# Optimization experiments

Measured on AMD Instinct MI355X. Metric: run time of the kernel, lower is better.

The kernel has to match this reference:

```python
import jax, jax.numpy as jnp
import numpy as np

K = 20  # hard-coded in Codebook.forward


def _renorm(x):
    # x / ||x||_2 along dim 1, matching torch renorm()
    return x / jnp.linalg.norm(x, axis=1, keepdims=True)


def setup_inputs() -> dict:
    key = jax.random.key(0)
    ks = jax.random.split(key, 6)
    B, N, D = 2048, 50000, 128
    z_rot = jax.random.normal(ks[0], (B, D), dtype=jnp.float32)
    z_trans = jax.random.normal(ks[1], (B, D), dtype=jnp.float32)
    # rotation codebook entries are pre-renormed in create_codetensors
    z_rot_book = _renorm(jax.random.normal(ks[2], (N, D), dtype=jnp.float32))
    z_trans_book = jax.random.normal(ks[3], (N, D), dtype=jnp.float32)
    rot_book = jax.random.uniform(ks[4], (N, 1), dtype=jnp.float32) * 360.0
    trans_book = jax.random.normal(ks[5], (N, 3), dtype=jnp.float32)
    return {
        "z_rot": z_rot,
        "z_trans": z_trans,
        "z_rot_book": z_rot_book,
        "z_trans_book": z_trans_book,
        "rot_book": rot_book,
        "trans_book": trans_book,
    }


def reference(z_rot, z_trans, z_rot_book, z_trans_book, rot_book, trans_book):
    # --- get_nearest_cosine ---
    zr = _renorm(z_rot)                                   # [B, D]
    cos = jnp.einsum("bd,nd->bn", zr, z_rot_book)        # [B, N]
    vals_cos, ind_cos = jax.lax.top_k(cos, K)             # [B, K]
    labels_rot = rot_book[ind_cos]                        # [B, K, 1]

    # --- get_nearest_euclidean ---
    # -(||z - b||^2) = -(||z||^2 - 2 z.b + ||b||^2); avoids the [B,N,D]
    # broadcasted intermediate the torch code materializes (same math).
    zq = jnp.sum(z_trans * z_trans, axis=1, keepdims=True)          # [B, 1]
    bq = jnp.sum(z_trans_book * z_trans_book, axis=1)               # [N]
    m2 = 2.0 * jnp.einsum("bd,nd->bn", z_trans, z_trans_book) - zq - bq[None, :]
    vals_euc, ind_euc = jax.lax.top_k(m2, K)              # [B, K]
    labels_trans = trans_book[ind_euc]                    # [B, K, 3]

    return vals_cos, ind_cos, labels_rot, vals_euc, ind_euc, labels_trans
```

## Files before the change

### kernel.cpp

```cpp
#include <hip/hip_runtime.h>
#include <cfloat>
#include <climits>
#include <math.h>

#define BB 2048
#define NN 50000
#define DD 128
#define KK 20

#define NSLICE 16
#define NSL 3125
#define NTILE 98
#define TAILV 21
#define LK 8
#define SLC 16
#define CAND 256
#define K1W 4

#define O_VC 0
#define O_IC 40960
#define O_LR 81920
#define O_VE 122880
#define O_IE 163840
#define O_LT 204800

#define WS_BBF   0
#define WS_BQ2   25690112
#define WS_CAND  25890112

#define BSTR 132

typedef short v8s __attribute__((ext_vector_type(8)));
typedef float v16f __attribute__((ext_vector_type(16)));

union U4V8 { uint4 u; v8s v; };

__device__ __forceinline__ unsigned int bf16rne(float f) {
    unsigned int x = __float_as_uint(f);
    return (x + 0x7FFFu + ((x >> 16) & 1u)) >> 16;
}
__device__ __forceinline__ unsigned int sortkey(float s) {
    unsigned int b = __float_as_uint(s);
    return b ^ ((unsigned int)((int)b >> 31) | 0x80000000u);
}
__device__ __forceinline__ unsigned int med3u(unsigned int a, unsigned int b, unsigned int c) {
    unsigned int d;
    asm("v_med3_u32 %0, %1, %2, %3" : "=v"(d) : "v"(a), "v"(b), "v"(c));
    return d;
}
__device__ __forceinline__ void ins8(unsigned int (&run)[LK], unsigned int k) {
    #pragma unroll
    for (int u = 0; u < LK - 1; u++) run[u] = med3u(k, run[u], run[u + 1]);
    run[LK - 1] = max(k, run[LK - 1]);
}
__device__ __forceinline__ void ce(unsigned int &a, unsigned int &b) {
    unsigned int lo = min(a, b);
    unsigned int hi = max(a, b);
    a = lo; b = hi;
}
__device__ __forceinline__ void merge8(unsigned int (&run)[LK], const unsigned int* s) {
    unsigned int m[8];
    #pragma unroll
    for (int i = 0; i < 8; i++) m[i] = max(run[i], s[7 - i]);
    ce(m[0],m[4]); ce(m[1],m[5]); ce(m[2],m[6]); ce(m[3],m[7]);
    ce(m[0],m[2]); ce(m[1],m[3]); ce(m[4],m[6]); ce(m[5],m[7]);
    ce(m[0],m[1]); ce(m[2],m[3]); ce(m[4],m[5]); ce(m[6],m[7]);
    #pragma unroll
    for (int i = 0; i < 8; i++) run[i] = m[i];
}

__global__ __launch_bounds__(256) void k_cvt2(const float* __restrict__ bR,
                                              const float* __restrict__ bT,
                                              unsigned int* __restrict__ Bbf,
                                              unsigned int* __restrict__ bq2)
{
    const int tile  = blockIdx.x;
    const int slice = blockIdx.y;
    const int task  = blockIdx.z;
    const int t = threadIdx.x;
    const float* __restrict__ src = task ? bT : bR;
    const float sc = task ? 2.f : 1.f;

    __shared__ float ps[4][64];

    unsigned int* tb = Bbf + (((size_t)(task * NSLICE + slice) * NTILE + tile) << 11);

    float partial = 0.f;
    #pragma unroll
    for (int half = 0; half < 2; half++) {
        const int x = t + half * 256;
        const int c = x & 31, hh = (x >> 5) & 1, q = x >> 6;
        const int es = slice * NSL + min(tile * 32 + c, NSL - 1);
        const float* p = src + (size_t)es * DD + q * 16 + hh * 8;
        float4 u0 = *reinterpret_cast<const float4*>(p);
        float4 u1 = *reinterpret_cast<const float4*>(p + 4);
        partial += u0.x * u0.x + u0.y * u0.y + u0.z * u0.z + u0.w * u0.w
                 + u1.x * u1.x + u1.y * u1.y + u1.z * u1.z + u1.w * u1.w;
        uint4 o;
        o.x = bf16rne(u0.x * sc) | (bf16rne(u0.y * sc) << 16);
        o.y = bf16rne(u0.z * sc) | (bf16rne(u0.w * sc) << 16);
        o.z = bf16rne(u1.x * sc) | (bf16rne(u1.y * sc) << 16);
        o.w = bf16rne(u1.z * sc) | (bf16rne(u1.w * sc) << 16);
        *reinterpret_cast<uint4*>(tb + (q << 8) + hh * 128 + c * 4) = o;
    }

    if (task) {
        ps[t >> 6][t & 63] = partial;
        __syncthreads();
        if (t < 32) {
            float sq = 0.f;
            #pragma unroll
            for (int w2 = 0; w2 < 4; w2++) sq += ps[w2][t] + ps[w2][t + 32];
            unsigned int hi = bf16rne(sq);
            float fhi = __uint_as_float(hi << 16);
            unsigned int lo = bf16rne(sq - fhi);
            const int e = slice * NSL + min(tile * 32 + t, NSL - 1);
            bq2[e] = (hi ^ 0x8000u) | ((lo ^ 0x8000u) << 16);
        }
    }
}

__global__ __launch_bounds__(256, 8) void k1_sel(
    const float* __restrict__ zR, const float* __restrict__ zT,
    const unsigned int* __restrict__ Bbf,
    const unsigned int* __restrict__ bq2,
    uint4* __restrict__ candU)
{
    const int slice = blockIdx.x;
    const int rg    = blockIdx.y;
    const int task  = blockIdx.z;
    const int w     = threadIdx.x >> 6;
    const int lane  = threadIdx.x & 63;
    const int col   = lane & 31;
    const int h     = lane >> 5;

    __shared__ uint4 zs[8][64];
    __shared__ unsigned int smk[K1W - 1][64][LK + 1];

    if (w == 0) {
        const float* zp = (task ? zT : zR) + (size_t)(rg * 32 + col) * DD;
        #pragma unroll
        for (int q = 0; q < 8; q++) {
            float4 u0 = *reinterpret_cast<const float4*>(zp + q * 16 + h * 8);
            float4 u1 = *reinterpret_cast<const float4*>(zp + q * 16 + h * 8 + 4);
            uint4 c;
            c.x = bf16rne(u0.x) | (bf16rne(u0.y) << 16);
            c.y = bf16rne(u0.z) | (bf16rne(u0.w) << 16);
            c.z = bf16rne(u1.x) | (bf16rne(u1.y) << 16);
            c.w = bf16rne(u1.z) | (bf16rne(u1.w) << 16);
            zs[q][lane] = c;
        }
    }
    U4V8 zf8; zf8.u = make_uint4(h == 0 ? 0x3F803F80u : 0u, 0u, 0u, 0u);
    __syncthreads();

    unsigned int run[LK];
    #pragma unroll
    for (int u = 0; u < LK; u++) run[u] = 0u;

    const int nbase0 = slice * NSL;
    const unsigned int* bp = Bbf + ((size_t)(task * NSLICE + slice) * NTILE << 11) + lane * 4;

#define TILE_BODY(TILE, TAIL)                                                          \
    {                                                                                  \
        asm volatile("" ::: "memory");   \
        const unsigned int* tb = bp + ((size_t)(TILE) << 11);                          \
        v16f acc = {0.f,0.f,0.f,0.f, 0.f,0.f,0.f,0.f,                                  \
                    0.f,0.f,0.f,0.f, 0.f,0.f,0.f,0.f};                                 \
        _Pragma("unroll")                                                              \
        for (int q = 0; q < 8; q++) {                                                  \
            U4V8 a; a.u = *reinterpret_cast<const uint4*>(tb + (q << 8));              \
            U4V8 z; z.u = zs[q][lane];                                                 \
            acc = __builtin_amdgcn_mfma_f32_32x32x16_bf16(a.v, z.v, acc, 0, 0, 0);     \
        }                                                                              \
        if (task) {                                                                    \
            int e = nbase0 + (TILE) * 32 + col;                                        \
            if (TAIL) e = min(e, nbase0 + NSL - 1);                                    \
            unsigned int bqp = bq2[e];                                                 \
            U4V8 a; a.u = make_uint4(h == 0 ? bqp : 0u, 0u, 0u, 0u);                   \
            acc = __builtin_amdgcn_mfma_f32_32x32x16_bf16(a.v, zf8.v, acc, 0, 0, 0);   \
        }                                                                              \
        const int nb = nbase0 + (TILE) * 32 + 4 * h;                                   \
        _Pragma("unroll")                                                              \
        for (int r = 0; r < 16; r++) {                                                 \
            const int pat = (r & 3) + 8 * (r >> 2);                                    \
            const int n = nb + pat;                                                    \
            unsigned int k = (sortkey(acc[r]) & 0xFFFF0000u) | (unsigned int)n;        \
            if (TAIL && (pat + 4 * h >= TAILV)) k = 0u;                                \
            ins8(run, k);                                                              \
        }                                                                              \
    }

    int tile = w;
    for (; tile < NTILE - 1; tile += K1W) TILE_BODY(tile, 0)
    if (tile == NTILE - 1) TILE_BODY(tile, 1)
#undef TILE_BODY

    if (w > 0) {
        #pragma unroll
        for (int u = 0; u < LK; u++) smk[w - 1][lane][u] = run[u];
    }
    __syncthreads();
    if (w == 0) {
        #pragma unroll
        for (int v = 0; v < K1W - 1; v++) {
            unsigned int s[LK];
            #pragma unroll
            for (int u = 0; u < LK; u++) s[u] = smk[v][lane][u];
            merge8(run, s);
        }

        uint4 o;
        o.x = (run[0] & 0xFFFFu) | ((run[1] & 0xFFFFu) << 16);
        o.y = (run[2] & 0xFFFFu) | ((run[3] & 0xFFFFu) << 16);
        o.z = (run[4] & 0xFFFFu) | ((run[5] & 0xFFFFu) << 16);
        o.w = (run[6] & 0xFFFFu) | ((run[7] & 0xFFFFu) << 16);
        const int row = rg * 32 + col;
        candU[((size_t)(task * BB + row) * NSLICE + slice) * 2 + h] = o;
    }
}

__global__ __launch_bounds__(256) void k2_final(
    const float* __restrict__ Zr, const float* __restrict__ Zt,
    const float* __restrict__ Br, const float* __restrict__ Bt,
    const float* __restrict__ rotB, const float* __restrict__ transB,
    const unsigned short* __restrict__ candU16,
    float* __restrict__ out)
{
    const int row = blockIdx.x;
    const int task = blockIdx.y;
    const int t = threadIdx.x;
    const float* __restrict__ Z  = task ? Zt : Zr;
    const float* __restrict__ Bk = task ? Bt : Br;

    __shared__ __align__(16) float zrow[DD];
    __shared__ int sel[CAND];
    __shared__ double dsum[CAND];
    __shared__ double sval[KK];
    __shared__ int sidx[KK];
    __shared__ float sv[CAND];
    __shared__ __align__(16) float buf[64 * BSTR];

    if (t < DD) zrow[t] = Z[(size_t)row * DD + t];
    sel[t] = (int)candU16[((size_t)task * BB + row) * CAND + t];
    __syncthreads();

    const int sr = t >> 2;
    const int sg = t & 3;

    for (int c = 0; c < 4; ++c) {
        {
            const int n = sel[c * 64 + sr];
            const float* src = Bk + (size_t)n * DD + sg * 32;
            float4 tmp[8];
            #pragma unroll
            for (int i = 0; i < 8; i++)
                tmp[i] = *reinterpret_cast<const float4*>(src + i * 4);
            #pragma unroll
            for (int i = 0; i < 8; i++)
                *reinterpret_cast<float4*>(&buf[sr * BSTR + sg * 32 + i * 4]) = tmp[i];
        }
        __syncthreads();

        if (task == 0) {
            #pragma unroll
            for (int sub = 0; sub < 2; sub++) {
                const int idx = c * 512 + sub * 256 + t;
                const int cnd = idx >> 3, part = idx & 7;
                const float* brow = &buf[(cnd - c * 64) * BSTR + part * 16];
                double dp = 0.0;
                #pragma unroll
                for (int q = 0; q < 4; q++) {
                    float4 b4 = *reinterpret_cast<const float4*>(brow + q * 4);
                    const int k = part * 16 + q * 4;
                    dp += (double)zrow[k + 0] * (double)b4.x + (double)zrow[k + 1] * (double)b4.y
                        + (double)zrow[k + 2] * (double)b4.z + (double)zrow[k + 3] * (double)b4.w;
                }
                dp += __shfl_xor(dp, 1, 64);
                dp += __shfl_xor(dp, 2, 64);
                dp += __shfl_xor(dp, 4, 64);
                if ((t & 7) == 0) dsum[cnd] = dp;
            }
        } else {
            const float* brow = &buf[sr * BSTR];
            float L = 0.f, rA = 0.f, rB = 0.f, qA = 0.f, qB = 0.f;
            #pragma unroll
            for (int c4 = 0; c4 < 32; c4++) {
                const float b = brow[c4 * 4 + sg];
                const float z = zrow[c4 * 4 + sg];
                L = __fadd_rn(L, __fmul_rn(z, b));
                if ((c4 & 1) == 0) {
                    rA = __fadd_rn(rA, __fmul_rn(b, b));
                    qA = __fadd_rn(qA, __fmul_rn(z, z));
                } else {
                    rB = __fadd_rn(rB, __fmul_rn(b, b));
                    qB = __fadd_rn(qB, __fmul_rn(z, z));
                }
            }
            float a2 = __fadd_rn(L, __shfl_xor(L, 2, 64));
            float dot = __fadd_rn(a2, __shfl_xor(a2, 1, 64));
            float s1 = __fadd_rn(rA, __shfl_xor(rA, 1, 64));
            float u1 = __fadd_rn(s1, __shfl_xor(s1, 2, 64));
            float s2 = __fadd_rn(rB, __shfl_xor(rB, 1, 64));
            float u2 = __fadd_rn(s2, __shfl_xor(s2, 2, 64));
            const float bqv = __fadd_rn(u1, u2);
            float s3 = __fadd_rn(qA, __shfl_xor(qA, 1, 64));
            float u3 = __fadd_rn(s3, __shfl_xor(s3, 2, 64));
            float s4 = __fadd_rn(qB, __shfl_xor(qB, 1, 64));
            float u4 = __fadd_rn(s4, __shfl_xor(s4, 2, 64));
            const float zqv = __fadd_rn(u3, u4);
            if (sg == 0)
                sv[c * 64 + sr] = __fsub_rn(__fsub_rn(__fmul_rn(2.0f, dot), zqv), bqv);
        }
        __syncthreads();
    }

    if (task == 0) {
        if (t < 64) {
            double zq = (double)zrow[t] * (double)zrow[t]
                      + (double)zrow[t + 64] * (double)zrow[t + 64];
            #pragma unroll
            for (int m = 1; m < 64; m <<= 1) zq += __shfl_xor(zq, m, 64);

            double s[4]; int ix[4];
            #pragma unroll
            for (int j = 0; j < 4; j++) {
                const int cc = t + 64 * j;
                s[j] = dsum[cc]; ix[j] = sel[cc];
            }

            for (int rd = 0; rd < KK; rd++) {
                double bs = s[0]; int bn = ix[0];
                #pragma unroll
                for (int j = 1; j < 4; j++)
                    if (s[j] > bs || (s[j] == bs && ix[j] < bn)) { bs = s[j]; bn = ix[j]; }
                #pragma unroll
                for (int m = 1; m < 64; m <<= 1) {
                    double os = __shfl_xor(bs, m, 64);
                    int on = __shfl_xor(bn, m, 64);
                    if (os > bs || (os == bs && on < bn)) { bs = os; bn = on; }
                }
                #pragma unroll
                for (int j = 0; j < 4; j++) if (ix[j] == bn) s[j] = -DBL_MAX;
                if (t == 0) { sval[rd] = bs; sidx[rd] = bn; }
            }
            if (t == 0) dsum[0] = zq;
        }
        __syncthreads();

        if (t < KK) {
            const double zq = dsum[0];
            const int n = sidx[t];
            const int o = row * KK + t;
            out[O_VC + o] = (float)(sval[t] / sqrt(zq));
            out[O_IC + o] = (float)n;
            out[O_LR + o] = rotB[n];
        }
    } else {
        if (t < 64) {
            float s[4]; int ix[4];
            #pragma unroll
            for (int j = 0; j < 4; j++) { s[j] = sv[t + 64 * j]; ix[j] = sel[t + 64 * j]; }

            for (int rd = 0; rd < KK; rd++) {
                float bs = s[0]; int bn = ix[0];
                #pragma unroll
                for (int j = 1; j < 4; j++)
                    if (s[j] > bs || (s[j] == bs && ix[j] < bn)) { bs = s[j]; bn = ix[j]; }
                #pragma unroll
                for (int m = 1; m < 64; m <<= 1) {
                    float os = __shfl_xor(bs, m, 64);
                    int on = __shfl_xor(bn, m, 64);
                    if (os > bs || (os == bs && on < bn)) { bs = os; bn = on; }
                }
                #pragma unroll
                for (int j = 0; j < 4; j++) if (ix[j] == bn) s[j] = -FLT_MAX;
                if (t == 0) {
                    const int o = row * KK + rd;
                    out[O_VE + o] = bs;
                    out[O_IE + o] = (float)bn;
                    const int o3 = O_LT + o * 3;
                    out[o3 + 0] = transB[bn * 3 + 0];
                    out[o3 + 1] = transB[bn * 3 + 1];
                    out[o3 + 2] = transB[bn * 3 + 2];
                }
            }
        }
    }
}

extern "C" void kernel_launch(void* const* d_in, const int* in_sizes, int n_in,
                              void* d_out, int out_size, void* d_ws, size_t ws_size,
                              hipStream_t stream) {
    const float* zR = (const float*)d_in[0];
    const float* zT = (const float*)d_in[1];
    const float* bR = (const float*)d_in[2];
    const float* bT = (const float*)d_in[3];
    const float* rotB = (const float*)d_in[4];
    const float* transB = (const float*)d_in[5];
    float* out = (float*)d_out;

    char* ws = (char*)d_ws;
    unsigned int* Bbf = (unsigned int*)(ws + WS_BBF);
    unsigned int* bq2 = (unsigned int*)(ws + WS_BQ2);
    uint4* candU = (uint4*)(ws + WS_CAND);

    k_cvt2<<<dim3(NTILE, NSLICE, 2), 256, 0, stream>>>(bR, bT, Bbf, bq2);
    k1_sel<<<dim3(NSLICE, 64, 2), 256, 0, stream>>>(zR, zT, Bbf, bq2, candU);
    k2_final<<<dim3(BB, 2), 256, 0, stream>>>(zR, zT, bR, bT, rotB, transB,
                                              (const unsigned short*)candU, out);
}
```

Baseline: 335.4 us.

## Split final rescoring into parallel rescore kernel and wave-sized top-K kernel

Replaces the single per-row final kernel with two kernels. The first rescores the 256 candidates per row across four blocks per row, reading codebook rows straight from global memory with no shared-memory staging or barriers. The second uses one 64-thread wave per row to pick the top-K from the rescored values kept in workspace. This is meant to raise parallelism and remove the serialized chunk loop and its syncs, at the cost of an extra launch and a global round trip for the scores. The scores go in the workspace region that held the bf16 codebook, which is dead by then.

```diff
diff --git a/kernel.cpp b/kernel.cpp
--- a/kernel.cpp
+++ b/kernel.cpp
@@ -27,8 +27,8 @@
 #define WS_BBF   0
 #define WS_BQ2   25690112
 #define WS_CAND  25890112
-
-#define BSTR 132
+#define WS_DSUM  0
+#define WS_SV    4194304
 
 typedef short v8s __attribute__((ext_vector_type(8)));
 typedef float v16f __attribute__((ext_vector_type(16)));
@@ -220,136 +220,119 @@
     }
 }
 
-__global__ __launch_bounds__(256) void k2_final(
+__global__ __launch_bounds__(256) void k2a_rescore(
     const float* __restrict__ Zr, const float* __restrict__ Zt,
     const float* __restrict__ Br, const float* __restrict__ Bt,
+    const unsigned short* __restrict__ candU16,
+    double* __restrict__ dsumW, float* __restrict__ svW)
+{
+    const int row   = blockIdx.x;
+    const int chunk = blockIdx.y;
+    const int task  = blockIdx.z;
+    const int t  = threadIdx.x;
+    const int sr = t >> 2;
+    const int sg = t & 3;
+    const int cidx = chunk * 64 + sr;
+    const int n = (int)candU16[((size_t)task * BB + row) * CAND + cidx];
+
+    if (task == 0) {
+        const float* brow = Br + (size_t)n * DD + sg * 32;
+        const float* zrow = Zr + (size_t)row * DD + sg * 32;
+        double dp = 0.0;
+        #pragma unroll
+        for (int q = 0; q < 8; q++) {
+            float4 b4 = *reinterpret_cast<const float4*>(brow + q * 4);
+            float4 z4 = *reinterpret_cast<const float4*>(zrow + q * 4);
+            dp += (double)z4.x * (double)b4.x + (double)z4.y * (double)b4.y
+                + (double)z4.z * (double)b4.z + (double)z4.w * (double)b4.w;
+        }
+        dp += __shfl_xor(dp, 1, 64);
+        dp += __shfl_xor(dp, 2, 64);
+        if (sg == 0) dsumW[(size_t)row * CAND + cidx] = dp;
+    } else {
+        const float* brow = Bt + (size_t)n * DD;
+        const float* zrow = Zt + (size_t)row * DD;
+        float L = 0.f, rA = 0.f, rB = 0.f, qA = 0.f, qB = 0.f;
+        #pragma unroll
+        for (int c4 = 0; c4 < 32; c4++) {
+            const float b = brow[c4 * 4 + sg];
+            const float z = zrow[c4 * 4 + sg];
+            L = __fadd_rn(L, __fmul_rn(z, b));
+            if ((c4 & 1) == 0) {
+                rA = __fadd_rn(rA, __fmul_rn(b, b));
+                qA = __fadd_rn(qA, __fmul_rn(z, z));
+            } else {
+                rB = __fadd_rn(rB, __fmul_rn(b, b));
+                qB = __fadd_rn(qB, __fmul_rn(z, z));
+            }
+        }
+        float a2 = __fadd_rn(L, __shfl_xor(L, 2, 64));
+        float dot = __fadd_rn(a2, __shfl_xor(a2, 1, 64));
+        float s1 = __fadd_rn(rA, __shfl_xor(rA, 1, 64));
+        float u1 = __fadd_rn(s1, __shfl_xor(s1, 2, 64));
+        float s2 = __fadd_rn(rB, __shfl_xor(rB, 1, 64));
+        float u2 = __fadd_rn(s2, __shfl_xor(s2, 2, 64));
+        const float bqv = __fadd_rn(u1, u2);
+        float s3 = __fadd_rn(qA, __shfl_xor(qA, 1, 64));
+        float u3 = __fadd_rn(s3, __shfl_xor(s3, 2, 64));
+        float s4 = __fadd_rn(qB, __shfl_xor(qB, 1, 64));
+        float u4 = __fadd_rn(s4, __shfl_xor(s4, 2, 64));
+        const float zqv = __fadd_rn(u3, u4);
+        if (sg == 0)
+            svW[(size_t)row * CAND + cidx] =
+                __fsub_rn(__fsub_rn(__fmul_rn(2.0f, dot), zqv), bqv);
+    }
+}
+
+__global__ __launch_bounds__(64) void k2b_final(
+    const float* __restrict__ Zr,
     const float* __restrict__ rotB, const float* __restrict__ transB,
     const unsigned short* __restrict__ candU16,
+    const double* __restrict__ dsumW, const float* __restrict__ svW,
     float* __restrict__ out)
 {
     const int row = blockIdx.x;
     const int task = blockIdx.y;
     const int t = threadIdx.x;
-    const float* __restrict__ Z  = task ? Zt : Zr;
-    const float* __restrict__ Bk = task ? Bt : Br;
-
-    __shared__ __align__(16) float zrow[DD];
-    __shared__ int sel[CAND];
-    __shared__ double dsum[CAND];
+
     __shared__ double sval[KK];
     __shared__ int sidx[KK];
-    __shared__ float sv[CAND];
-    __shared__ __align__(16) float buf[64 * BSTR];
-
-    if (t < DD) zrow[t] = Z[(size_t)row * DD + t];
-    sel[t] = (int)candU16[((size_t)task * BB + row) * CAND + t];
-    __syncthreads();
-
-    const int sr = t >> 2;
-    const int sg = t & 3;
-
-    for (int c = 0; c < 4; ++c) {
-        {
-            const int n = sel[c * 64 + sr];
-            const float* src = Bk + (size_t)n * DD + sg * 32;
-            float4 tmp[8];
-            #pragma unroll
-            for (int i = 0; i < 8; i++)
-                tmp[i] = *reinterpret_cast<const float4*>(src + i * 4);
-            #pragma unroll
-            for (int i = 0; i < 8; i++)
-                *reinterpret_cast<float4*>(&buf[sr * BSTR + sg * 32 + i * 4]) = tmp[i];
+
+    const unsigned short* selp = candU16 + ((size_t)task * BB + row) * CAND;
+
+    if (task == 0) {
+        const float z0 = Zr[(size_t)row * DD + t];
+        const float z1 = Zr[(size_t)row * DD + t + 64];
+        double zq = (double)z0 * (double)z0 + (double)z1 * (double)z1;
+        #pragma unroll
+        for (int m = 1; m < 64; m <<= 1) zq += __shfl_xor(zq, m, 64);
+
+        double s[4]; int ix[4];
+        #pragma unroll
+        for (int j = 0; j < 4; j++) {
+            const int cc = t + 64 * j;
+            s[j] = dsumW[(size_t)row * CAND + cc];
+            ix[j] = (int)selp[cc];
+        }
+
+        for (int rd = 0; rd < KK; rd++) {
+            double bs = s[0]; int bn = ix[0];
+            #pragma unroll
+            for (int j = 1; j < 4; j++)
+                if (s[j] > bs || (s[j] == bs && ix[j] < bn)) { bs = s[j]; bn = ix[j]; }
+            #pragma unroll
+            for (int m = 1; m < 64; m <<= 1) {
+                double os = __shfl_xor(bs, m, 64);
+                int on = __shfl_xor(bn, m, 64);
+                if (os > bs || (os == bs && on < bn)) { bs = os; bn = on; }
+            }
+            #pragma unroll
+            for (int j = 0; j < 4; j++) if (ix[j] == bn) s[j] = -DBL_MAX;
+            if (t == 0) { sval[rd] = bs; sidx[rd] = bn; }
         }
         __syncthreads();
 
-        if (task == 0) {
-            #pragma unroll
-            for (int sub = 0; sub < 2; sub++) {
-                const int idx = c * 512 + sub * 256 + t;
-                const int cnd = idx >> 3, part = idx & 7;
-                const float* brow = &buf[(cnd - c * 64) * BSTR + part * 16];
-                double dp = 0.0;
-                #pragma unroll
-                for (int q = 0; q < 4; q++) {
-                    float4 b4 = *reinterpret_cast<const float4*>(brow + q * 4);
-                    const int k = part * 16 + q * 4;
-                    dp += (double)zrow[k + 0] * (double)b4.x + (double)zrow[k + 1] * (double)b4.y
-                        + (double)zrow[k + 2] * (double)b4.z + (double)zrow[k + 3] * (double)b4.w;
-                }
-                dp += __shfl_xor(dp, 1, 64);
-                dp += __shfl_xor(dp, 2, 64);
-                dp += __shfl_xor(dp, 4, 64);
-                if ((t & 7) == 0) dsum[cnd] = dp;
-            }
-        } else {
-            const float* brow = &buf[sr * BSTR];
-            float L = 0.f, rA = 0.f, rB = 0.f, qA = 0.f, qB = 0.f;
-            #pragma unroll
-            for (int c4 = 0; c4 < 32; c4++) {
-                const float b = brow[c4 * 4 + sg];
-                const float z = zrow[c4 * 4 + sg];
-                L = __fadd_rn(L, __fmul_rn(z, b));
-                if ((c4 & 1) == 0) {
-                    rA = __fadd_rn(rA, __fmul_rn(b, b));
-                    qA = __fadd_rn(qA, __fmul_rn(z, z));
-                } else {
-                    rB = __fadd_rn(rB, __fmul_rn(b, b));
-                    qB = __fadd_rn(qB, __fmul_rn(z, z));
-                }
-            }
-            float a2 = __fadd_rn(L, __shfl_xor(L, 2, 64));
-            float dot = __fadd_rn(a2, __shfl_xor(a2, 1, 64));
-            float s1 = __fadd_rn(rA, __shfl_xor(rA, 1, 64));
-            float u1 = __fadd_rn(s1, __shfl_xor(s1, 2, 64));
-            float s2 = __fadd_rn(rB, __shfl_xor(rB, 1, 64));
-            float u2 = __fadd_rn(s2, __shfl_xor(s2, 2, 64));
-            const float bqv = __fadd_rn(u1, u2);
-            float s3 = __fadd_rn(qA, __shfl_xor(qA, 1, 64));
-            float u3 = __fadd_rn(s3, __shfl_xor(s3, 2, 64));
-            float s4 = __fadd_rn(qB, __shfl_xor(qB, 1, 64));
-            float u4 = __fadd_rn(s4, __shfl_xor(s4, 2, 64));
-            const float zqv = __fadd_rn(u3, u4);
-            if (sg == 0)
-                sv[c * 64 + sr] = __fsub_rn(__fsub_rn(__fmul_rn(2.0f, dot), zqv), bqv);
-        }
-        __syncthreads();
-    }
-
-    if (task == 0) {
-        if (t < 64) {
-            double zq = (double)zrow[t] * (double)zrow[t]
-                      + (double)zrow[t + 64] * (double)zrow[t + 64];
-            #pragma unroll
-            for (int m = 1; m < 64; m <<= 1) zq += __shfl_xor(zq, m, 64);
-
-            double s[4]; int ix[4];
-            #pragma unroll
-            for (int j = 0; j < 4; j++) {
-                const int cc = t + 64 * j;
-                s[j] = dsum[cc]; ix[j] = sel[cc];
-            }
-
-            for (int rd = 0; rd < KK; rd++) {
-                double bs = s[0]; int bn = ix[0];
-                #pragma unroll
-                for (int j = 1; j < 4; j++)
-                    if (s[j] > bs || (s[j] == bs && ix[j] < bn)) { bs = s[j]; bn = ix[j]; }
-                #pragma unroll
-                for (int m = 1; m < 64; m <<= 1) {
-                    double os = __shfl_xor(bs, m, 64);
-                    int on = __shfl_xor(bn, m, 64);
-                    if (os > bs || (os == bs && on < bn)) { bs = os; bn = on; }
-                }
-                #pragma unroll
-                for (int j = 0; j < 4; j++) if (ix[j] == bn) s[j] = -DBL_MAX;
-                if (t == 0) { sval[rd] = bs; sidx[rd] = bn; }
-            }
-            if (t == 0) dsum[0] = zq;
-        }
-        __syncthreads();
-
         if (t < KK) {
-            const double zq = dsum[0];
             const int n = sidx[t];
             const int o = row * KK + t;
             out[O_VC + o] = (float)(sval[t] / sqrt(zq));
@@ -357,33 +340,35 @@
             out[O_LR + o] = rotB[n];
         }
     } else {
-        if (t < 64) {
-            float s[4]; int ix[4];
-            #pragma unroll
-            for (int j = 0; j < 4; j++) { s[j] = sv[t + 64 * j]; ix[j] = sel[t + 64 * j]; }
-
-            for (int rd = 0; rd < KK; rd++) {
-                float bs = s[0]; int bn = ix[0];
-                #pragma unroll
-                for (int j = 1; j < 4; j++)
-                    if (s[j] > bs || (s[j] == bs && ix[j] < bn)) { bs = s[j]; bn = ix[j]; }
-                #pragma unroll
-                for (int m = 1; m < 64; m <<= 1) {
-                    float os = __shfl_xor(bs, m, 64);
-                    int on = __shfl_xor(bn, m, 64);
-                    if (os > bs || (os == bs && on < bn)) { bs = os; bn = on; }
-                }
-                #pragma unroll
-                for (int j = 0; j < 4; j++) if (ix[j] == bn) s[j] = -FLT_MAX;
-                if (t == 0) {
-                    const int o = row * KK + rd;
-                    out[O_VE + o] = bs;
-                    out[O_IE + o] = (float)bn;
-                    const int o3 = O_LT + o * 3;
-                    out[o3 + 0] = transB[bn * 3 + 0];
-                    out[o3 + 1] = transB[bn * 3 + 1];
-                    out[o3 + 2] = transB[bn * 3 + 2];
-                }
+        float s[4]; int ix[4];
+        #pragma unroll
+        for (int j = 0; j < 4; j++) {
+            const int cc = t + 64 * j;
+            s[j] = svW[(size_t)row * CAND + cc];
+            ix[j] = (int)selp[cc];
+        }
+
+        for (int rd = 0; rd < KK; rd++) {
+            float bs = s[0]; int bn = ix[0];
+            #pragma unroll
+            for (int j = 1; j < 4; j++)
+                if (s[j] > bs || (s[j] == bs && ix[j] < bn)) { bs = s[j]; bn = ix[j]; }
+            #pragma unroll
+            for (int m = 1; m < 64; m <<= 1) {
+                float os = __shfl_xor(bs, m, 64);
+                int on = __shfl_xor(bn, m, 64);
+                if (os > bs || (os == bs && on < bn)) { bs = os; bn = on; }
+            }
+            #pragma unroll
+            for (int j = 0; j < 4; j++) if (ix[j] == bn) s[j] = -FLT_MAX;
+            if (t == 0) {
+                const int o = row * KK + rd;
+                out[O_VE + o] = bs;
+                out[O_IE + o] = (float)bn;
+                const int o3 = O_LT + o * 3;
+                out[o3 + 0] = transB[bn * 3 + 0];
+                out[o3 + 1] = transB[bn * 3 + 1];
+                out[o3 + 2] = transB[bn * 3 + 2];
             }
         }
     }
@@ -404,9 +389,15 @@
     unsigned int* Bbf = (unsigned int*)(ws + WS_BBF);
     unsigned int* bq2 = (unsigned int*)(ws + WS_BQ2);
     uint4* candU = (uint4*)(ws + WS_CAND);
+    double* dsumW = (double*)(ws + WS_DSUM);
+    float* svW = (float*)(ws + WS_SV);
 
     k_cvt2<<<dim3(NTILE, NSLICE, 2), 256, 0, stream>>>(bR, bT, Bbf, bq2);
     k1_sel<<<dim3(NSLICE, 64, 2), 256, 0, stream>>>(zR, zT, Bbf, bq2, candU);
-    k2_final<<<dim3(BB, 2), 256, 0, stream>>>(zR, zT, bR, bT, rotB, transB,
-                                              (const unsigned short*)candU, out);
-}
+    k2a_rescore<<<dim3(BB, 4, 2), 256, 0, stream>>>(zR, zT, bR, bT,
+                                                    (const unsigned short*)candU,
+                                                    dsumW, svW);
+    k2b_final<<<dim3(BB, 2), 64, 0, stream>>>(zR, rotB, transB,
+                                              (const unsigned short*)candU,
+                                              dsumW, svW, out);
+}
```

Result: faster. 328.4 us (-2.1%).
